# Optimization experiments

Measured on AMD Instinct MI355X. Metric: run time of the kernel, lower is better.

The kernel has to match this reference:

```python
import jax, jax.numpy as jnp
import numpy as np

H, D = 8, 8            # heads, per-head dim (hid_dim = 64)
HID = H * D
L = 6                  # HGTConv layers
NI, NV = 32768, 131072 # num 'instr' / 'var' nodes (batch_size == NI)
E_VV, E_VI, E_IV = 1048576, 524288, 524288
INV_SQRT_D = float(1.0 / np.sqrt(D))


def _seg_softmax(logits, seg, n):
    # softmax over edges grouped by destination node (PyG softmax semantics)
    m = jax.ops.segment_max(logits, seg, num_segments=n)
    m = jnp.where(jnp.isfinite(m), m, 0.0)
    e = jnp.exp(logits - m[seg])
    s = jax.ops.segment_sum(e, seg, num_segments=n)
    return e / (s[seg] + 1e-16)


def _edge_msg(k_src, v_src, q_dst, arel, mrel, prel, src, dst, n_dst):
    # relation-specific transforms: [N_src,H,D] x [H,D,D] -> [N_src,H,D]
    k_rel = jnp.einsum('nhd,hde->nhe', k_src, arel)
    v_rel = jnp.einsum('nhd,hde->nhe', v_src, mrel)
    alpha = jnp.einsum('ehd,ehd->eh', q_dst[dst], k_rel[src]) * prel * INV_SQRT_D  # [E,H]
    w = _seg_softmax(alpha, dst, n_dst)
    return jax.ops.segment_sum(v_rel[src] * w[:, :, None], dst, num_segments=n_dst)


def _kqv(x, Wk, Wq, Wv, bk, bq, bv, n):
    k = (x @ Wk.T + bk).reshape(n, H, D)
    q = (x @ Wq.T + bq).reshape(n, H, D)
    v = (x @ Wv.T + bv).reshape(n, H, D)
    return k, q, v


def _forward(x_instr, x_var,
             Wk_i, Wq_i, Wv_i, Wa_i, bk_i, bq_i, bv_i, ba_i, skip_i,
             Wk_v, Wq_v, Wv_v, Wa_v, bk_v, bq_v, bv_v, ba_v, skip_v,
             arel_vv, mrel_vv, prel_vv, arel_vi, mrel_vi, prel_vi,
             arel_iv, mrel_iv, prel_iv,
             Wqkv, bqkv, Wo, bo,
             mw0, mb0, mw1, mb1, mw2, mb2, mw3, mb3, mw4, mb4, mw5, mb5,
             src_vv, dst_vv, src_vi, dst_vi, src_iv, dst_iv):
    xi, xv = x_instr, x_var
    outs = []
    for l in range(L):
        k_i, q_i, v_i = _kqv(xi, Wk_i[l], Wq_i[l], Wv_i[l], bk_i[l], bq_i[l], bv_i[l], NI)
        k_v, q_v, v_v = _kqv(xv, Wk_v[l], Wq_v[l], Wv_v[l], bk_v[l], bq_v[l], bv_v[l], NV)
        # per-edge-type attention softmax + scatter-sum, then sum over edge types (group='sum')
        agg_v = (_edge_msg(k_v, v_v, q_v, arel_vv[l], mrel_vv[l], prel_vv[l], src_vv, dst_vv, NV)
                 + _edge_msg(k_i, v_i, q_v, arel_iv[l], mrel_iv[l], prel_iv[l], src_iv, dst_iv, NV))
        agg_i = _edge_msg(k_v, v_v, q_i, arel_vi[l], mrel_vi[l], prel_vi[l], src_vi, dst_vi, NI)
        o_i = jax.nn.gelu(agg_i.reshape(NI, HID), approximate=False) @ Wa_i[l].T + ba_i[l]
        b_i = jax.nn.sigmoid(skip_i[l])
        xi = b_i * o_i + (1.0 - b_i) * xi
        o_v = jax.nn.gelu(agg_v.reshape(NV, HID), approximate=False) @ Wa_v[l].T + ba_v[l]
        b_v = jax.nn.sigmoid(skip_v[l])
        xv = b_v * o_v + (1.0 - b_v) * xv
        if l > 0:
            outs.append(xi)
    # jumping-knowledge MultiheadAttention over the L-1 stacked layer outputs
    x = jnp.stack(outs)                        # [S, NI, HID], S = L-1 = 5
    S = x.shape[0]
    qkv = x @ Wqkv.T + bqkv                    # [S, NI, 3*HID]
    q, k, v = jnp.split(qkv, 3, axis=-1)
    q = q.reshape(S, NI, H, D)
    k = k.reshape(S, NI, H, D)
    v = v.reshape(S, NI, H, D)
    sc = jnp.einsum('snhd,tnhd->nhst', q, k) * INV_SQRT_D
    w = jax.nn.softmax(sc, axis=-1)
    o = jnp.einsum('nhst,tnhd->snhd', w, v).reshape(S, NI, HID)
    o = o @ Wo.T + bo
    out = o.sum(axis=0)                        # [NI, HID]; batch_size == NI so view is identity
    for W, b in ((mw0, mb0), (mw1, mb1), (mw2, mb2), (mw3, mb3), (mw4, mb4)):
        out = jax.nn.gelu(out @ W.T + b, approximate=False)
    out = out @ mw5.T + mb5                    # [NI, 1]
    return out[:, 0]


def setup_inputs() -> dict:
    key = jax.random.key(0)
    ks = iter(jax.random.split(key, 64))
    def nrm(shape, scale=1.0):
        return jax.random.normal(next(ks), shape, dtype=jnp.float32) * scale
    d = {}
    d['x_instr'] = nrm((NI, HID))
    d['x_var'] = nrm((NV, HID))
    for t in ('i', 'v'):
        for p in ('Wk', 'Wq', 'Wv', 'Wa'):
            d[f'{p}_{t}'] = nrm((L, HID, HID), (2.0 / HID) ** 0.5)
        for p in ('bk', 'bq', 'bv', 'ba'):
            d[f'{p}_{t}'] = jnp.zeros((L, HID), jnp.float32)
        d[f'skip_{t}'] = jnp.ones((L,), jnp.float32)
    for e in ('vv', 'vi', 'iv'):
        d[f'arel_{e}'] = nrm((L, H, D, D), (1.0 / D) ** 0.5)
        d[f'mrel_{e}'] = nrm((L, H, D, D), (1.0 / D) ** 0.5)
        d[f'prel_{e}'] = jnp.ones((L, H), jnp.float32)
    d['Wqkv'] = nrm((3 * HID, HID), (2.0 / HID) ** 0.5)
    d['bqkv'] = jnp.zeros((3 * HID,), jnp.float32)
    d['Wo'] = nrm((HID, HID), (2.0 / HID) ** 0.5)
    d['bo'] = jnp.zeros((HID,), jnp.float32)
    dims = [64, 32, 16, 8, 4, 2, 1]
    for i in range(6):
        d[f'mw{i}'] = nrm((dims[i + 1], dims[i]), (2.0 / dims[i]) ** 0.5)
        d[f'mb{i}'] = jnp.zeros((dims[i + 1],), jnp.float32)
    d['src_vv'] = jax.random.randint(next(ks), (E_VV,), 0, NV, dtype=jnp.int32).astype(jnp.int64)
    d['dst_vv'] = jax.random.randint(next(ks), (E_VV,), 0, NV, dtype=jnp.int32).astype(jnp.int64)
    d['src_vi'] = jax.random.randint(next(ks), (E_VI,), 0, NV, dtype=jnp.int32).astype(jnp.int64)
    d['dst_vi'] = jax.random.randint(next(ks), (E_VI,), 0, NI, dtype=jnp.int32).astype(jnp.int64)
    d['src_iv'] = jax.random.randint(next(ks), (E_IV,), 0, NI, dtype=jnp.int32).astype(jnp.int64)
    d['dst_iv'] = jax.random.randint(next(ks), (E_IV,), 0, NV, dtype=jnp.int32).astype(jnp.int64)
    return d


def reference(x_instr, x_var,
              Wk_i, Wq_i, Wv_i, Wa_i, bk_i, bq_i, bv_i, ba_i, skip_i,
              Wk_v, Wq_v, Wv_v, Wa_v, bk_v, bq_v, bv_v, ba_v, skip_v,
              arel_vv, mrel_vv, prel_vv, arel_vi, mrel_vi, prel_vi,
              arel_iv, mrel_iv, prel_iv,
              Wqkv, bqkv, Wo, bo,
              mw0, mb0, mw1, mb1, mw2, mb2, mw3, mb3, mw4, mb4, mw5, mb5,
              src_vv, dst_vv, src_vi, dst_vi, src_iv, dst_iv):
    return _forward(x_instr, x_var,
                    Wk_i, Wq_i, Wv_i, Wa_i, bk_i, bq_i, bv_i, ba_i, skip_i,
                    Wk_v, Wq_v, Wv_v, Wa_v, bk_v, bq_v, bv_v, ba_v, skip_v,
                    arel_vv, mrel_vv, prel_vv, arel_vi, mrel_vi, prel_vi,
                    arel_iv, mrel_iv, prel_iv,
                    Wqkv, bqkv, Wo, bo,
                    mw0, mb0, mw1, mb1, mw2, mb2, mw3, mb3, mw4, mb4, mw5, mb5,
                    src_vv, dst_vv, src_vi, dst_vi, src_iv, dst_iv)
```

## Files before the change

kernel.cpp:

```cpp
#include <hip/hip_runtime.h>
#include <cmath>

typedef _Float16 f16_t;
typedef __attribute__((ext_vector_type(8))) short short8;
typedef __attribute__((ext_vector_type(8))) _Float16 half8;
typedef __attribute__((ext_vector_type(4))) float f32x4;
typedef _Float16 h2v __attribute__((ext_vector_type(2)));
typedef _Float16 h8 __attribute__((ext_vector_type(8)));
typedef float f2 __attribute__((ext_vector_type(2)));

#define NI_N 32768
#define NV_N 131072
#define E_VV 1048576
#define E_VI 524288
#define E_IV 524288
#define NT_N (NV_N+NV_N+NI_N)
#define ET_N (E_VV+E_IV+E_VI)
#define SC_WIN 4
#define LOG2E 1.4426950408889634f
#define CHV 192
#define CHI 64
#define CHQ 256
#define EPAD 68

__device__ __forceinline__ float gelu_f(float x){ return 0.5f*x*(1.0f+erff(x*0.7071067811865476f)); }

__device__ __forceinline__ void splitf16(float v, short& hi, short& lo){
  f16_t h=(f16_t)v;
  hi=__builtin_bit_cast(short,h);
  f16_t l=(f16_t)(v-(float)h);
  lo=__builtin_bit_cast(short,l);
}
__device__ __forceinline__ f32x4 mfma16(short8 a, short8 b, f32x4 c){
  return __builtin_amdgcn_mfma_f32_16x16x32_f16(__builtin_bit_cast(half8,a),__builtin_bit_cast(half8,b),c,0,0,0);
}
__device__ __forceinline__ float fexp2(float x){
#if __has_builtin(__builtin_amdgcn_exp2f)
  return __builtin_amdgcn_exp2f(x);
#else
  return exp2f(x);
#endif
}
__device__ __forceinline__ float ldval(const float* p){ return *p; }
__device__ __forceinline__ float ldval(const f16_t* p){ return (float)*p; }
__device__ __forceinline__ void stval(float* p,float v){ *p=v; }
__device__ __forceinline__ void stval(f16_t* p,float v){ *p=(f16_t)v; }

__global__ __launch_bounds__(256) void k_hist3(const int* __restrict__ dvv,const int* __restrict__ div_,
    const int* __restrict__ dvi,int* __restrict__ cnt){
  int i=blockIdx.x*256+threadIdx.x;
  if(i<E_VV) atomicAdd(&cnt[dvv[i]],1);
  else if(i<E_VV+E_IV) atomicAdd(&cnt[NV_N+div_[i-E_VV]],1);
  else atomicAdd(&cnt[2*NV_N+dvi[i-E_VV-E_IV]],1);
}
__global__ __launch_bounds__(512) void k_scan1(const int* __restrict__ cnt,int N,int* __restrict__ rp,int* __restrict__ bsum){
  __shared__ int sh[512];
  int i=blockIdx.x*512+threadIdx.x;
  int v=(i<N)?cnt[i]:0;
  sh[threadIdx.x]=v; __syncthreads();
  for(int off=1;off<512;off<<=1){
    int t=(threadIdx.x>=(unsigned)off)?sh[threadIdx.x-off]:0; __syncthreads();
    sh[threadIdx.x]+=t; __syncthreads();
  }
  if(i<N) rp[i]=sh[threadIdx.x]-v;
  if(threadIdx.x==511) bsum[blockIdx.x]=sh[511];
}
__global__ __launch_bounds__(1024) void k_scan2(const int* __restrict__ bsum,int* __restrict__ boff,int nb){
  __shared__ int sh[1024];
  int t=threadIdx.x;
  int v=(t<nb)?bsum[t]:0;
  sh[t]=v; __syncthreads();
  for(int off=1;off<1024;off<<=1){
    int x=(t>=(unsigned)off)?sh[t-off]:0; __syncthreads();
    sh[t]+=x; __syncthreads();
  }
  if(t<nb) boff[t]=sh[t]-v;
  if(t==1023) boff[nb]=sh[1023];
}
__global__ __launch_bounds__(512) void k_scan3(int* __restrict__ rp,const int* __restrict__ boff,int* __restrict__ cur,int N,int nb){
  int i=blockIdx.x*512+threadIdx.x;
  if(i<N){ int v=rp[i]+boff[i>>9]; rp[i]=v; cur[i]=v; }
  if(i==0) rp[N]=boff[nb];
}
__global__ __launch_bounds__(256) void k_scatter3w(const int* __restrict__ svv,const int* __restrict__ dvv,
    const int* __restrict__ siv,const int* __restrict__ div_,
    const int* __restrict__ svi,const int* __restrict__ dvi,
    int* __restrict__ cur,int* __restrict__ esrc,int dlo,int dhi){
  int i=blockIdx.x*256+threadIdx.x;
  int d,s;
  if(i<E_VV){ d=dvv[i]; if(d<dlo||d>=dhi) return; s=svv[i]*320; }
  else if(i<E_VV+E_IV){ int j=i-E_VV; d=NV_N+div_[j]; if(d<dlo||d>=dhi) return; s=siv[j]*192; }
  else { int j=i-E_VV-E_IV; d=2*NV_N+dvi[j]; if(d<dlo||d>=dhi) return; s=svi[j]*320; }
  int p=atomicAdd(&cur[d],1); esrc[p]=s;
}

__global__ __launch_bounds__(256) void k_castx(const float* __restrict__ xi_in,const float* __restrict__ xv_in,
    f16_t* __restrict__ xi,f16_t* __restrict__ xv){
  int i=blockIdx.x*256+threadIdx.x;
  if(i<NI_N*64) xi[i]=(f16_t)xi_in[i];
  else { int j=i-NI_N*64; xv[j]=(f16_t)xv_in[j]; }
}

struct FoldArgs{
  const float *Wk_i,*Wq_i,*Wv_i,*bk_i,*bq_i,*bv_i;
  const float *Wk_v,*Wq_v,*Wv_v,*bk_v,*bq_v,*bv_v;
  const float *arel_vv,*mrel_vv,*prel_vv,*arel_vi,*mrel_vi,*prel_vi,*arel_iv,*mrel_iv,*prel_iv;
  const float *Wa_i,*Wa_v;
  short *fwh_var,*fwl_var,*fwh_ins,*fwl_ins,*wah_i,*wal_i,*wah_v,*wal_v;
  float *fwb_var,*fwb_ins;
};
__global__ __launch_bounds__(256) void k_fold6(FoldArgs fa){
  int gid=blockIdx.x*256+threadIdx.x;
  if(gid>=6*640*64) return;
  int l=gid/(640*64);
  int rem=gid-l*640*64;
  int r=rem>>6, c=rem&63;
  if(r>=512){
    int ro=r&63;
    const float* W=(r<576)?fa.Wa_i:fa.Wa_v;
    short *sh=((r<576)?fa.wah_i:fa.wah_v)+l*4096, *sl=((r<576)?fa.wal_i:fa.wal_v)+l*4096;
    short h,lo; splitf16(W[l*4096+ro*64+c],h,lo);
    sh[ro*64+c]=h; sl[ro*64+c]=lo;
    return;
  }
  const float *W,*B,*rel=nullptr,*prl=nullptr;
  short *sh,*sl; float *fwb; int orow; bool isq=false;
  if(r<320){
    sh=fa.fwh_var+l*320*64; sl=fa.fwl_var+l*320*64; fwb=fa.fwb_var+l*320; orow=r;
    if(r<64){ W=fa.Wq_v; B=fa.bq_v; isq=true; }
    else if(r<128){ W=fa.Wk_v; B=fa.bk_v; rel=fa.arel_vv; prl=fa.prel_vv; }
    else if(r<192){ W=fa.Wv_v; B=fa.bv_v; rel=fa.mrel_vv; }
    else if(r<256){ W=fa.Wk_v; B=fa.bk_v; rel=fa.arel_vi; prl=fa.prel_vi; }
    else         { W=fa.Wv_v; B=fa.bv_v; rel=fa.mrel_vi; }
  }else{
    int rr=r-320; sh=fa.fwh_ins+l*192*64; sl=fa.fwl_ins+l*192*64; fwb=fa.fwb_ins+l*192; orow=rr;
    if(rr<64){ W=fa.Wq_i; B=fa.bq_i; isq=true; }
    else if(rr<128){ W=fa.Wk_i; B=fa.bk_i; rel=fa.arel_iv; prl=fa.prel_iv; }
    else           { W=fa.Wv_i; B=fa.bv_i; rel=fa.mrel_iv; }
  }
  int d=orow&63;
  float val,bval;
  if(!rel){
    val=W[l*4096+d*64+c]; bval=B[l*64+d];
  }else{
    int h=d>>3, e=d&7;
    float s=prl?prl[l*8+h]*0.3535533905932738f:1.0f;
    float acc=0.f,bacc=0.f;
    #pragma unroll
    for(int dd=0;dd<8;dd++){
      float rv=rel[l*512+h*64+dd*8+e];
      acc += W[l*4096+(h*8+dd)*64+c]*rv;
      bacc+= B[l*64+h*8+dd]*rv;
    }
    val=acc*s; bval=bacc*s;
  }
  if(isq){ val*=LOG2E; bval*=LOG2E; }
  short h2q,lo2; splitf16(val,h2q,lo2);
  sh[orow*64+c]=h2q; sl[orow*64+c]=lo2;
  if(c==0) fwb[orow]=bval;
}

__global__ __launch_bounds__(256) void k_split2(const float* __restrict__ W,int n,short* __restrict__ hi,short* __restrict__ lo){
  int i=blockIdx.x*256+threadIdx.x;
  if(i<n){ short h,l2; splitf16(W[i],h,l2); hi[i]=h; lo[i]=l2; }
}

__device__ __forceinline__ void colres_body(const f16_t* __restrict__ A,int nrb,
    const short* __restrict__ Bh,const short* __restrict__ Bl,
    const float* __restrict__ bias,f16_t* __restrict__ out,int octot,int ocol0,
    int c,int CH,int wave,int lane,int m,int quad,f16_t (*rep)[72])
{
  short8 bhi[4][2], blo[4][2]; float bb[4];
  #pragma unroll
  for(int ot=0;ot<4;ot++){
    size_t o=(size_t)(ocol0+ot*16+m)*64+quad*8;
    bhi[ot][0]=*(const short8*)(Bh+o);    bhi[ot][1]=*(const short8*)(Bh+o+32);
    blo[ot][0]=*(const short8*)(Bl+o);    blo[ot][1]=*(const short8*)(Bl+o+32);
    bb[ot]=bias[ocol0+ot*16+m];
  }
  int rr0=lane>>3, seg=lane&7;
  for(int rb=c;rb<nrb;rb+=CH){
    int row0=rb*64+wave*16;
    const f16_t* ap=A+(size_t)(row0+m)*64+quad*8;
    short8 a0=*(const short8*)(const void*)ap;
    short8 a1=*(const short8*)(const void*)(ap+32);
    f32x4 acc[4];
    #pragma unroll
    for(int ot=0;ot<4;ot++){ f32x4 t={bb[ot],bb[ot],bb[ot],bb[ot]}; acc[ot]=t; }
    #pragma unroll
    for(int ot=0;ot<4;ot++){
      acc[ot]=mfma16(a0,blo[ot][0],acc[ot]);
      acc[ot]=mfma16(a0,bhi[ot][0],acc[ot]);
      acc[ot]=mfma16(a1,blo[ot][1],acc[ot]);
      acc[ot]=mfma16(a1,bhi[ot][1],acc[ot]);
    }
    #pragma unroll
    for(int ot=0;ot<4;ot++)
      #pragma unroll
      for(int r=0;r<4;r++)
        rep[quad*4+r][ot*16+m]=(f16_t)acc[ot][r];
    #pragma unroll
    for(int it=0;it<2;it++){
      int rr=it*8+rr0;
      h8 vals=*(const h8*)&rep[rr][seg*8];
      *(h8*)(out+(size_t)(row0+rr)*octot+ocol0+seg*8)=vals;
    }
  }
}

__global__ __launch_bounds__(256) void k_colres_feat(const f16_t* __restrict__ Av,const f16_t* __restrict__ Ai,
    const short* __restrict__ Bvh,const short* __restrict__ Bvl,const float* __restrict__ biasv,
    const short* __restrict__ Bih,const short* __restrict__ Bil,const float* __restrict__ biasi,
    f16_t* __restrict__ outv,f16_t* __restrict__ outi)
{
  __shared__ f16_t rep[4][16][72];
  const int wave=threadIdx.x>>6, lane=threadIdx.x&63;
  const int m=lane&15, quad=lane>>4;
  int bx=blockIdx.x;
  if(bx<5*CHV){
    int pan=bx/CHV, c=bx%CHV;
    colres_body(Av,NV_N/64,Bvh,Bvl,biasv,outv,320,pan*64,c,CHV,wave,lane,m,quad,rep[wave]);
  }else{
    bx-=5*CHV;
    int pan=bx/CHI, c=bx%CHI;
    colres_body(Ai,NI_N/64,Bih,Bil,biasi,outi,192,pan*64,c,CHI,wave,lane,m,quad,rep[wave]);
  }
}

__global__ __launch_bounds__(256) void k_colres1(const f16_t* __restrict__ A,int nrb,
    const short* __restrict__ Bh,const short* __restrict__ Bl,
    const float* __restrict__ bias,f16_t* __restrict__ out,int octot,int CH)
{
  __shared__ f16_t rep[4][16][72];
  const int wave=threadIdx.x>>6, lane=threadIdx.x&63;
  const int m=lane&15, quad=lane>>4;
  int pan=blockIdx.x/CH, c=blockIdx.x%CH;
  colres_body(A,nrb,Bh,Bl,bias,out,octot,pan*64,c,CH,wave,lane,m,quad,rep[wave]);
}

template<typename AT, typename OT>
__device__ __forceinline__ void gemm_body(const AT* __restrict__ A,int row0,
    const short* __restrict__ Bh,const short* __restrict__ Bl,
    const float* __restrict__ bias,float bias_scale,
    OT* __restrict__ out,int octot,int ocol0,int npanels,int m,int quad,int lane,
    f16_t (*rep)[72])
{
  const AT* ap=A+(size_t)(row0+m)*64+quad*8;
  constexpr bool AF16 = (sizeof(AT)==2);
  short8 ahi[2], alo[2];
  if constexpr(AF16){
    #pragma unroll
    for(int kf=0;kf<2;kf++) ahi[kf]=*(const short8*)(const void*)(ap+kf*32);
  }else{
    #pragma unroll
    for(int kf=0;kf<2;kf++){
      short8 th,tl;
      #pragma unroll
      for(int j=0;j<8;j++){ short h,l2; splitf16(ldval(&ap[kf*32+j]),h,l2); th[j]=h; tl[j]=l2; }
      ahi[kf]=th; alo[kf]=tl;
    }
  }
  for(int pan=0;pan<npanels;pan++){
    int colbase=pan*64;
    short8 bhi[4][2], blo[4][2];
    #pragma unroll
    for(int ot=0;ot<4;ot++){
      size_t o=(size_t)(colbase+ot*16+m)*64+quad*8;
      #pragma unroll
      for(int kf=0;kf<2;kf++){
        bhi[ot][kf]=*(const short8*)(Bh+o+kf*32);
        blo[ot][kf]=*(const short8*)(Bl+o+kf*32);
      }
    }
    f32x4 acc[4];
    #pragma unroll
    for(int ot=0;ot<4;ot++){
      float bv=bias[colbase+ot*16+m]*bias_scale;
      acc[ot][0]=bv; acc[ot][1]=bv; acc[ot][2]=bv; acc[ot][3]=bv;
    }
    #pragma unroll
    for(int ot=0;ot<4;ot++){
      #pragma unroll
      for(int kf=0;kf<2;kf++){
        if constexpr(!AF16) acc[ot]=mfma16(alo[kf],bhi[ot][kf],acc[ot]);
        acc[ot]=mfma16(ahi[kf],blo[ot][kf],acc[ot]);
        acc[ot]=mfma16(ahi[kf],bhi[ot][kf],acc[ot]);
      }
    }
    if constexpr(sizeof(OT)==2){
      #pragma unroll
      for(int ot=0;ot<4;ot++)
        #pragma unroll
        for(int r=0;r<4;r++)
          rep[quad*4+r][ot*16+m]=(f16_t)acc[ot][r];
      #pragma unroll
      for(int it=0;it<2;it++){
        int rr=it*8+(lane>>3), seg=lane&7;
        h8 vals=*(const h8*)&rep[rr][seg*8];
        *(h8*)(out+(size_t)(row0+rr)*octot+ocol0+colbase+seg*8)=vals;
      }
    }else{
      #pragma unroll
      for(int ot=0;ot<4;ot++){
        int col=ocol0+colbase+ot*16+m;
        #pragma unroll
        for(int r=0;r<4;r++){
          int row=row0+quad*4+r;
          stval(&out[(size_t)row*octot+col],acc[ot][r]);
        }
      }
    }
  }
}

template<typename AT, typename OT>
__global__ __launch_bounds__(256) void k_gemm64p(const AT* __restrict__ A,int N,
    const short* __restrict__ Bh,const short* __restrict__ Bl,
    const float* __restrict__ bias,float bias_scale,
    OT* __restrict__ out,int octot,int ocol0,int npanels)
{
  __shared__ f16_t rep[4][16][72];
  const int wave=threadIdx.x>>6, lane=threadIdx.x&63;
  const int m=lane&15, quad=lane>>4;
  const int row0=blockIdx.x*64+wave*16;
  if(row0>=N) return;
  gemm_body<AT,OT>(A,row0,Bh,Bl,bias,bias_scale,out,octot,ocol0,npanels,m,quad,lane,rep[wave]);
}

__global__ __launch_bounds__(256) void k_update2(const f16_t* __restrict__ agg_i,const f16_t* __restrict__ agg_v,
    const short* __restrict__ wah_i,const short* __restrict__ wal_i,
    const short* __restrict__ wah_v,const short* __restrict__ wal_v,
    const float* __restrict__ ba_i,const float* __restrict__ ba_v,
    const float* __restrict__ skip_i,const float* __restrict__ skip_v,
    f16_t* __restrict__ x_i,f16_t* __restrict__ x_v,
    f16_t* __restrict__ outs,int nbi)
{
  __shared__ f16_t rep[4][16][72];
  const int wave=threadIdx.x>>6, lane=threadIdx.x&63;
  const int m=lane&15, quad=lane>>4;
  const bool isI=(int)blockIdx.x<nbi;
  const int row0=(isI?blockIdx.x:(blockIdx.x-nbi))*64+wave*16;
  const f16_t* agg=isI?agg_i:agg_v;
  const short* Wah=isI?wah_i:wah_v;
  const short* Wal=isI?wal_i:wal_v;
  const float* ba=isI?ba_i:ba_v;
  const float* skip=isI?skip_i:skip_v;
  f16_t* x=isI?x_i:x_v;
  f16_t* oo=isI?outs:nullptr;
  f16_t (*R)[72]=rep[wave];
  short8 bhi[4][2], blo[4][2];
  #pragma unroll
  for(int ot=0;ot<4;ot++){
    size_t o=(size_t)(ot*16+m)*64+quad*8;
    #pragma unroll
    for(int kf=0;kf<2;kf++){
      bhi[ot][kf]=*(const short8*)(Wah+o+kf*32);
      blo[ot][kf]=*(const short8*)(Wal+o+kf*32);
    }
  }
  const f16_t* ap=agg+(size_t)(row0+m)*64+quad*8;
  short8 ahi[2], alo[2];
  #pragma unroll
  for(int kf=0;kf<2;kf++){
    short8 th,tl;
    #pragma unroll
    for(int j=0;j<8;j++){ short h,l2; splitf16(gelu_f((float)ap[kf*32+j]),h,l2); th[j]=h; tl[j]=l2; }
    ahi[kf]=th; alo[kf]=tl;
  }
  int rr0=lane>>3, seg=lane&7;
  h8 x0=*(const h8*)(x+(size_t)(row0+rr0)*64+seg*8);
  h8 x1=*(const h8*)(x+(size_t)(row0+8+rr0)*64+seg*8);
  *(h8*)&R[rr0][seg*8]=x0;
  *(h8*)&R[8+rr0][seg*8]=x1;
  f32x4 acc[4];
  #pragma unroll
  for(int ot=0;ot<4;ot++){
    float bv=ba[ot*16+m];
    acc[ot][0]=bv; acc[ot][1]=bv; acc[ot][2]=bv; acc[ot][3]=bv;
  }
  #pragma unroll
  for(int ot=0;ot<4;ot++){
    #pragma unroll
    for(int kf=0;kf<2;kf++){
      acc[ot]=mfma16(alo[kf],bhi[ot][kf],acc[ot]);
      acc[ot]=mfma16(ahi[kf],blo[ot][kf],acc[ot]);
      acc[ot]=mfma16(ahi[kf],bhi[ot][kf],acc[ot]);
    }
  }
  float s=1.0f/(1.0f+__expf(-skip[0]));
  #pragma unroll
  for(int ot=0;ot<4;ot++){
    int col=ot*16+m;
    #pragma unroll
    for(int r=0;r<4;r++){
      int row=quad*4+r;
      float xn=s*acc[ot][r]+(1.0f-s)*(float)R[row][col];
      R[row][col]=(f16_t)xn;
    }
  }
  h8 o0=*(const h8*)&R[rr0][seg*8];
  h8 o1=*(const h8*)&R[8+rr0][seg*8];
  *(h8*)(x+(size_t)(row0+rr0)*64+seg*8)=o0;
  *(h8*)(x+(size_t)(row0+8+rr0)*64+seg*8)=o1;
  if(oo){
    *(h8*)(oo+(size_t)(row0+rr0)*64+seg*8)=o0;
    *(h8*)(oo+(size_t)(row0+8+rr0)*64+seg*8)=o1;
  }
}

__device__ __forceinline__ float dot8(h8 k,h2v q0,h2v q1,h2v q2,h2v q3){
#if __has_builtin(__builtin_amdgcn_fdot2)
  float p=__builtin_amdgcn_fdot2((h2v){k[0],k[1]},q0,0.f,false);
  p=__builtin_amdgcn_fdot2((h2v){k[2],k[3]},q1,p,false);
  p=__builtin_amdgcn_fdot2((h2v){k[4],k[5]},q2,p,false);
  p=__builtin_amdgcn_fdot2((h2v){k[6],k[7]},q3,p,false);
  return p;
#else
  return (float)k[0]*(float)q0[0]+(float)k[1]*(float)q0[1]
        +(float)k[2]*(float)q1[0]+(float)k[3]*(float)q1[1]
        +(float)k[4]*(float)q2[0]+(float)k[5]*(float)q2[1]
        +(float)k[6]*(float)q3[0]+(float)k[7]*(float)q3[1];
#endif
}

__device__ __forceinline__ float edge_agg_eh(const int* __restrict__ rp,const int* __restrict__ es,
    const f16_t* __restrict__ sf,int koff,int voff,int n,int e_slot,int h,int lane,
    h2v q0,h2v q1,h2v q2,h2v q3,float* __restrict__ L)
{
  int b=__builtin_amdgcn_readfirstlane(rp[n]);
  int e=__builtin_amdgcn_readfirstlane(rp[n+1]);
  if(b==e) return 0.f;
  float m=-1e30f, ls=0.f;
  f2 A0={0.f,0.f},A1={0.f,0.f},A2={0.f,0.f},A3={0.f,0.f};
  const int hb=h*8;
  for(int i=b;i<e;i+=8){
    int eidx=i+e_slot;
    bool valid=eidx<e;
    int ec=valid?eidx:(e-1);
    int off=es[ec];
    const f16_t* kp=sf+(size_t)(unsigned)off+koff+hb;
    h8 kv=*(const h8*)kp;
    h8 vv=*(const h8*)(sf+(size_t)(unsigned)off+voff+hb);
    float p=dot8(kv,q0,q1,q2,q3);
    float d=p-m;
    if(__builtin_expect(d>8.f,0)){
      float sc=fexp2(-d);
      ls*=sc;
      f2 S={sc,sc};
      A0*=S; A1*=S; A2*=S; A3*=S;
      m=p; d=0.f;
    }
    float w=valid?fexp2(d):0.f;
    ls+=w;
    f2 W={w,w};
    A0+=W*(f2){(float)vv[0],(float)vv[1]};
    A1+=W*(f2){(float)vv[2],(float)vv[3]};
    A2+=W*(f2){(float)vv[4],(float)vv[5]};
    A3+=W*(f2){(float)vv[6],(float)vv[7]};
  }
  float mall=fmaxf(m,__shfl_xor(m,8));
  mall=fmaxf(mall,__shfl_xor(mall,16));
  mall=fmaxf(mall,__shfl_xor(mall,32));
  float scl=fexp2(m-mall);
  ls*=scl;
  float lsall=ls+__shfl_xor(ls,8);
  lsall+=__shfl_xor(lsall,16);
  lsall+=__shfl_xor(lsall,32);
  f2 S2={scl,scl};
  A0*=S2; A1*=S2; A2*=S2; A3*=S2;
  float* wp=L+e_slot*EPAD+hb;
  *(f32x4*)wp=(f32x4){A0[0],A0[1],A1[0],A1[1]};
  *(f32x4*)(wp+4)=(f32x4){A2[0],A2[1],A3[0],A3[1]};
  __asm__ volatile("s_waitcnt lgkmcnt(0)" ::: "memory");
  float r=0.f;
  #pragma unroll
  for(int ee=0;ee<8;ee++) r+=L[ee*EPAD+lane];
  float lsr=__shfl(lsall,lane>>3);
  return r/(lsr+1e-16f);
}

__global__ __launch_bounds__(256) void k_edge_all(const int* __restrict__ rp_all,const int* __restrict__ es,
    const f16_t* __restrict__ var_feat,const f16_t* __restrict__ ins_feat,
    f16_t* __restrict__ agg_v,f16_t* __restrict__ agg_i,int nbv)
{
  __shared__ float lds[4][8*EPAD];
  int wave=threadIdx.x>>6, lane=threadIdx.x&63;
  int e_slot=lane>>3, h=lane&7;
  float* L=lds[wave];
  if((int)blockIdx.x<nbv){
    int n=blockIdx.x*4+wave;
    const f16_t* qp=var_feat+(size_t)n*320+h*8;
    h8 qv=*(const h8*)qp;
    h2v q0={qv[0],qv[1]},q1={qv[2],qv[3]},q2={qv[4],qv[5]},q3={qv[6],qv[7]};
    float r1=edge_agg_eh(rp_all,es,var_feat,64,128,n,e_slot,h,lane,q0,q1,q2,q3,L);
    float r2=edge_agg_eh(rp_all+NV_N,es,ins_feat,64,128,n,e_slot,h,lane,q0,q1,q2,q3,L);
    agg_v[(size_t)n*64+lane]=(f16_t)(r1+r2);
  }else{
    int n=(blockIdx.x-nbv)*4+wave;
    const f16_t* qp=ins_feat+(size_t)n*192+h*8;
    h8 qv=*(const h8*)qp;
    h2v q0={qv[0],qv[1]},q1={qv[2],qv[3]},q2={qv[4],qv[5]},q3={qv[6],qv[7]};
    float r=edge_agg_eh(rp_all+2*NV_N,es,var_feat,192,256,n,e_slot,h,lane,q0,q1,q2,q3,L);
    agg_i[(size_t)n*64+lane]=(f16_t)r;
  }
}

__global__ __launch_bounds__(256) void k_jk(const f16_t* __restrict__ qkv,float* __restrict__ osum,int n_nodes){
  int wave=threadIdx.x>>6, lane=threadIdx.x&63;
  int n=blockIdx.x*4+wave;
  if(n>=n_nodes) return;
  float q[5],k[5],v[5];
  #pragma unroll
  for(int s=0;s<5;s++){
    const f16_t* p=qkv+((size_t)s*n_nodes+n)*192;
    q[s]=(float)p[lane]; k[s]=(float)p[64+lane]; v[s]=(float)p[128+lane];
  }
  float sc[5][5];
  #pragma unroll
  for(int s=0;s<5;s++)
    #pragma unroll
    for(int t=0;t<5;t++){
      float x=q[s]*k[t];
      x+=__shfl_xor(x,1); x+=__shfl_xor(x,2); x+=__shfl_xor(x,4);
      sc[s][t]=x*0.3535533905932738f;
    }
  float os=0.f;
  #pragma unroll
  for(int s=0;s<5;s++){
    float m=sc[s][0];
    #pragma unroll
    for(int t=1;t<5;t++) m=fmaxf(m,sc[s][t]);
    float den=0.f, acc=0.f;
    #pragma unroll
    for(int t=0;t<5;t++){ float e=__expf(sc[s][t]-m); den+=e; acc+=e*v[t]; }
    os+=acc/den;
  }
  osum[(size_t)n*64+lane]=os;
}

struct MlpArgs{ const float *w0,*b0,*w1,*b1,*w2,*b2,*w3,*b3,*w4,*b4,*w5,*b5; };
__global__ __launch_bounds__(256) void k_mlp(const float* __restrict__ in,MlpArgs ma,float* __restrict__ out,int N){
  __shared__ float sw0[2048],sb0[32],sw1[512],sb1[16],sw2[128],sb2[8],sw3[32],sb3[4],sw4[8],sb4[2],sw5[2],sb5[1];
  for(int i=threadIdx.x;i<2048;i+=256) sw0[i]=ma.w0[i];
  for(int i=threadIdx.x;i<512;i+=256)  sw1[i]=ma.w1[i];
  if(threadIdx.x<128) sw2[threadIdx.x]=ma.w2[threadIdx.x];
  if(threadIdx.x<32){ sb0[threadIdx.x]=ma.b0[threadIdx.x]; sw3[threadIdx.x]=ma.w3[threadIdx.x]; }
  if(threadIdx.x<16) sb1[threadIdx.x]=ma.b1[threadIdx.x];
  if(threadIdx.x<8){ sb2[threadIdx.x]=ma.b2[threadIdx.x]; sw4[threadIdx.x]=ma.w4[threadIdx.x]; }
  if(threadIdx.x<4) sb3[threadIdx.x]=ma.b3[threadIdx.x];
  if(threadIdx.x<2){ sb4[threadIdx.x]=ma.b4[threadIdx.x]; sw5[threadIdx.x]=ma.w5[threadIdx.x]; }
  if(threadIdx.x==0) sb5[0]=ma.b5[0];
  __syncthreads();
  int n=blockIdx.x*256+threadIdx.x;
  if(n>=N) return;
  float a[64];
  const f32x4* p4=(const f32x4*)(in+(size_t)n*64);
  #pragma unroll
  for(int j=0;j<16;j++){ f32x4 t=p4[j]; a[4*j]=t[0]; a[4*j+1]=t[1]; a[4*j+2]=t[2]; a[4*j+3]=t[3]; }
  float h1[32];
  #pragma unroll
  for(int o=0;o<32;o++){ float s=sb0[o];
    #pragma unroll
    for(int c=0;c<64;c++) s+=a[c]*sw0[o*64+c];
    h1[o]=gelu_f(s); }
  float h2q[16];
  #pragma unroll
  for(int o=0;o<16;o++){ float s=sb1[o];
    #pragma unroll
    for(int c=0;c<32;c++) s+=h1[c]*sw1[o*32+c];
    h2q[o]=gelu_f(s); }
  float h3[8];
  #pragma unroll
  for(int o=0;o<8;o++){ float s=sb2[o];
    #pragma unroll
    for(int c=0;c<16;c++) s+=h2q[c]*sw2[o*16+c];
    h3[o]=gelu_f(s); }
  float h4[4];
  #pragma unroll
  for(int o=0;o<4;o++){ float s=sb3[o];
    #pragma unroll
    for(int c=0;c<8;c++) s+=h3[c]*sw3[o*8+c];
    h4[o]=gelu_f(s); }
  float h5[2];
  #pragma unroll
  for(int o=0;o<2;o++){ float s=sb4[o];
    #pragma unroll
    for(int c=0;c<4;c++) s+=h4[c]*sw4[o*4+c];
    h5[o]=gelu_f(s); }
  float r=sb5[0]+h5[0]*sw5[0]+h5[1]*sw5[1];
  out[n]=r;
}

extern "C" void kernel_launch(void* const* d_in,const int* in_sizes,int n_in,
                              void* d_out,int out_size,void* d_ws,size_t ws_size,
                              hipStream_t stream){
  (void)in_sizes;(void)n_in;(void)out_size;(void)ws_size;
  const float* x_instr=(const float*)d_in[0];
  const float* x_var  =(const float*)d_in[1];
  const float* ba_i=(const float*)d_in[9];
  const float* skip_i=(const float*)d_in[10];
  const float* ba_v=(const float*)d_in[18];
  const float* skip_v=(const float*)d_in[19];
  const float* Wqkv=(const float*)d_in[29];
  const float* bqkv=(const float*)d_in[30];
  const float* Wo=(const float*)d_in[31];
  const float* bo=(const float*)d_in[32];
  const int* src_vv=(const int*)d_in[45];
  const int* dst_vv=(const int*)d_in[46];
  const int* src_vi=(const int*)d_in[47];
  const int* dst_vi=(const int*)d_in[48];
  const int* src_iv=(const int*)d_in[49];
  const int* dst_iv=(const int*)d_in[50];

  char* w=(char*)d_ws;
  auto alloc=[&](size_t b)->char*{ char* p=w; w+=(b+255)&~(size_t)255; return p; };
  int* rp_all=(int*)alloc((size_t)(NT_N+1)*4);
  int* cnt_all=(int*)alloc((size_t)NT_N*4);
  int* cur_all=(int*)alloc((size_t)NT_N*4);
  int* bsum =(int*)alloc(640*4);
  int* boff =(int*)alloc(640*4);
  int* esrc_all=(int*)alloc((size_t)ET_N*4);
  short* fwh_var=(short*)alloc((size_t)6*320*64*2);
  short* fwl_var=(short*)alloc((size_t)6*320*64*2);
  float* fwb_var=(float*)alloc((size_t)6*320*4);
  short* fwh_ins=(short*)alloc((size_t)6*192*64*2);
  short* fwl_ins=(short*)alloc((size_t)6*192*64*2);
  float* fwb_ins=(float*)alloc((size_t)6*192*4);
  short* wah_i=(short*)alloc((size_t)6*64*64*2);
  short* wal_i=(short*)alloc((size_t)6*64*64*2);
  short* wah_v=(short*)alloc((size_t)6*64*64*2);
  short* wal_v=(short*)alloc((size_t)6*64*64*2);
  short* qkvh=(short*)alloc(192*64*2);
  short* qkvl=(short*)alloc(192*64*2);
  short* woh=(short*)alloc(64*64*2);
  short* wol=(short*)alloc(64*64*2);
  f16_t* outs=(f16_t*)alloc((size_t)5*NI_N*64*2);
  char* arena=alloc((size_t)146800640);
  f16_t*  xv      =(f16_t*)(arena);
  f16_t*  xi      =(f16_t*)(arena+16777216);
  f16_t*  var_feat=(f16_t*)(arena+20971520);
  f16_t*  ins_feat=(f16_t*)(arena+104857600);
  f16_t*  agg_v   =(f16_t*)(arena+117440512);
  f16_t*  agg_i   =(f16_t*)(arena+134217728);
  f16_t*  qkv    =(f16_t*)(arena);
  float*  osum   =(float*)(arena+67108864);
  float*  out_jk =(float*)(arena+75497472);

  hipMemsetAsync(cnt_all,0,(size_t)NT_N*4,stream);
  k_hist3<<<ET_N/256,256,0,stream>>>(dst_vv,dst_iv,dst_vi,cnt_all);
  int nb=NT_N/512;
  k_scan1<<<nb,512,0,stream>>>(cnt_all,NT_N,rp_all,bsum);
  k_scan2<<<1,1024,0,stream>>>(bsum,boff,nb);
  k_scan3<<<nb,512,0,stream>>>(rp_all,boff,cur_all,NT_N,nb);
  for(int wdx=0;wdx<SC_WIN;wdx++){
    int dlo=wdx*(NT_N/SC_WIN), dhi=(wdx+1)*(NT_N/SC_WIN);
    k_scatter3w<<<ET_N/256,256,0,stream>>>(src_vv,dst_vv,src_iv,dst_iv,src_vi,dst_vi,cur_all,esrc_all,dlo,dhi);
  }

  k_castx<<<(NI_N*64+NV_N*64)/256,256,0,stream>>>(x_instr,x_var,xi,xv);

  k_split2<<<(192*64+255)/256,256,0,stream>>>(Wqkv,192*64,qkvh,qkvl);
  k_split2<<<(64*64+255)/256,256,0,stream>>>(Wo,64*64,woh,wol);

  FoldArgs fa;
  fa.Wk_i=(const float*)d_in[2]; fa.Wq_i=(const float*)d_in[3]; fa.Wv_i=(const float*)d_in[4];
  fa.bk_i=(const float*)d_in[6]; fa.bq_i=(const float*)d_in[7]; fa.bv_i=(const float*)d_in[8];
  fa.Wk_v=(const float*)d_in[11]; fa.Wq_v=(const float*)d_in[12]; fa.Wv_v=(const float*)d_in[13];
  fa.bk_v=(const float*)d_in[15]; fa.bq_v=(const float*)d_in[16]; fa.bv_v=(const float*)d_in[17];
  fa.arel_vv=(const float*)d_in[20]; fa.mrel_vv=(const float*)d_in[21]; fa.prel_vv=(const float*)d_in[22];
  fa.arel_vi=(const float*)d_in[23]; fa.mrel_vi=(const float*)d_in[24]; fa.prel_vi=(const float*)d_in[25];
  fa.arel_iv=(const float*)d_in[26]; fa.mrel_iv=(const float*)d_in[27]; fa.prel_iv=(const float*)d_in[28];
  fa.Wa_i=(const float*)d_in[5]; fa.Wa_v=(const float*)d_in[14];
  fa.fwh_var=fwh_var; fa.fwl_var=fwl_var; fa.fwh_ins=fwh_ins; fa.fwl_ins=fwl_ins;
  fa.wah_i=wah_i; fa.wal_i=wal_i; fa.wah_v=wah_v; fa.wal_v=wal_v;
  fa.fwb_var=fwb_var; fa.fwb_ins=fwb_ins;
  k_fold6<<<(6*640*64)/256,256,0,stream>>>(fa);

  for(int l=0;l<6;l++){
    k_colres_feat<<<5*CHV+3*CHI,256,0,stream>>>(xv,xi,
        fwh_var+(size_t)l*320*64,fwl_var+(size_t)l*320*64,fwb_var+l*320,
        fwh_ins+(size_t)l*192*64,fwl_ins+(size_t)l*192*64,fwb_ins+l*192,
        var_feat,ins_feat);
    k_edge_all<<<NV_N/4+NI_N/4,256,0,stream>>>(rp_all,esrc_all,var_feat,ins_feat,agg_v,agg_i,NV_N/4);
    k_update2<<<NI_N/64+NV_N/64,256,0,stream>>>(agg_i,agg_v,
        wah_i+(size_t)l*4096,wal_i+(size_t)l*4096,wah_v+(size_t)l*4096,wal_v+(size_t)l*4096,
        ba_i+l*64,ba_v+l*64,skip_i+l,skip_v+l,xi,xv,
        (l>0)?(outs+(size_t)(l-1)*NI_N*64):nullptr,NI_N/64);
  }

  k_colres1<<<3*CHQ,256,0,stream>>>(outs,5*NI_N/64,qkvh,qkvl,bqkv,qkv,192,CHQ);
  k_jk<<<NI_N/4,256,0,stream>>>(qkv,osum,NI_N);
  k_gemm64p<float,float><<<NI_N/64,256,0,stream>>>(osum,NI_N,woh,wol,bo,5.0f,out_jk,64,0,1);
  MlpArgs ma;
  ma.w0=(const float*)d_in[33]; ma.b0=(const float*)d_in[34];
  ma.w1=(const float*)d_in[35]; ma.b1=(const float*)d_in[36];
  ma.w2=(const float*)d_in[37]; ma.b2=(const float*)d_in[38];
  ma.w3=(const float*)d_in[39]; ma.b3=(const float*)d_in[40];
  ma.w4=(const float*)d_in[41]; ma.b4=(const float*)d_in[42];
  ma.w5=(const float*)d_in[43]; ma.b5=(const float*)d_in[44];
  k_mlp<<<NI_N/256,256,0,stream>>>(out_jk,ma,(float*)d_out,NI_N);
}
```

Before: 1.542 ms.

## Software-pipeline edge gathers and hoist first-chunk loads in edge aggregation kernel

Restructures the per-destination edge loop so the next chunk's edge-source index is prefetched while the current chunk is processed. The first chunk's key/value vectors for both var-destination relations are loaded up front, so their latencies overlap. It also replaces the conditional online-softmax rescale with a branch-free max/rescale per step, and halves the scatter window count in preprocessing. The cost is more registers and extra exp work per edge, which could reduce occupancy.

```diff
diff --git a/kernel.cpp b/kernel.cpp
--- a/kernel.cpp
+++ b/kernel.cpp
@@ -16,7 +16,7 @@
 #define E_IV 524288
 #define NT_N (NV_N+NV_N+NI_N)
 #define ET_N (E_VV+E_IV+E_VI)
-#define SC_WIN 4
+#define SC_WIN 2
 #define LOG2E 1.4426950408889634f
 #define CHV 192
 #define CHI 64
@@ -423,40 +423,52 @@
 #endif
 }
 
-__device__ __forceinline__ float edge_agg_eh(const int* __restrict__ rp,const int* __restrict__ es,
-    const f16_t* __restrict__ sf,int koff,int voff,int n,int e_slot,int h,int lane,
-    h2v q0,h2v q1,h2v q2,h2v q3,float* __restrict__ L)
+__device__ __forceinline__ float edge_body(int b,int e,const int* __restrict__ es,
+    const f16_t* __restrict__ sf,int koff,int e_slot,int lane,
+    h2v q0,h2v q1,h2v q2,h2v q3,float* __restrict__ L,h8 pk,h8 pv)
 {
-  int b=__builtin_amdgcn_readfirstlane(rp[n]);
-  int e=__builtin_amdgcn_readfirstlane(rp[n+1]);
-  if(b==e) return 0.f;
+  if(b>=e) return 0.f;
   float m=-1e30f, ls=0.f;
   f2 A0={0.f,0.f},A1={0.f,0.f},A2={0.f,0.f},A3={0.f,0.f};
-  const int hb=h*8;
-  for(int i=b;i<e;i+=8){
-    int eidx=i+e_slot;
-    bool valid=eidx<e;
-    int ec=valid?eidx:(e-1);
-    int off=es[ec];
+  const int hb=(lane&7)*8;
+  int off=0;
+  if(b+8<e){ int ec=b+8+e_slot; ec=ec<e?ec:e-1; off=es[ec]; }
+  {
+    bool valid=(b+e_slot)<e;
+    float p=dot8(pk,q0,q1,q2,q3);
+    p=valid?p:-1e30f;
+    float mn=fmaxf(m,p);
+    float sc=fexp2(m-mn);
+    float w=valid?fexp2(p-mn):0.f;
+    ls=fmaf(ls,sc,w);
+    f2 S={sc,sc},W={w,w};
+    A0=A0*S+W*(f2){(float)pv[0],(float)pv[1]};
+    A1=A1*S+W*(f2){(float)pv[2],(float)pv[3]};
+    A2=A2*S+W*(f2){(float)pv[4],(float)pv[5]};
+    A3=A3*S+W*(f2){(float)pv[6],(float)pv[7]};
+    m=mn;
+  }
+  for(int i=b+8;i<e;i+=8){
+    int inext=i+8;
+    int offn=0;
+    if(inext<e){ int ec=inext+e_slot; ec=ec<e?ec:e-1; offn=es[ec]; }
     const f16_t* kp=sf+(size_t)(unsigned)off+koff+hb;
     h8 kv=*(const h8*)kp;
-    h8 vv=*(const h8*)(sf+(size_t)(unsigned)off+voff+hb);
+    h8 vv=*(const h8*)(kp+64);
+    bool valid=(i+e_slot)<e;
     float p=dot8(kv,q0,q1,q2,q3);
-    float d=p-m;
-    if(__builtin_expect(d>8.f,0)){
-      float sc=fexp2(-d);
-      ls*=sc;
-      f2 S={sc,sc};
-      A0*=S; A1*=S; A2*=S; A3*=S;
-      m=p; d=0.f;
-    }
-    float w=valid?fexp2(d):0.f;
-    ls+=w;
-    f2 W={w,w};
-    A0+=W*(f2){(float)vv[0],(float)vv[1]};
-    A1+=W*(f2){(float)vv[2],(float)vv[3]};
-    A2+=W*(f2){(float)vv[4],(float)vv[5]};
-    A3+=W*(f2){(float)vv[6],(float)vv[7]};
+    p=valid?p:-1e30f;
+    float mn=fmaxf(m,p);
+    float sc=fexp2(m-mn);
+    float w=valid?fexp2(p-mn):0.f;
+    ls=fmaf(ls,sc,w);
+    f2 S={sc,sc},W={w,w};
+    A0=A0*S+W*(f2){(float)vv[0],(float)vv[1]};
+    A1=A1*S+W*(f2){(float)vv[2],(float)vv[3]};
+    A2=A2*S+W*(f2){(float)vv[4],(float)vv[5]};
+    A3=A3*S+W*(f2){(float)vv[6],(float)vv[7]};
+    m=mn;
+    off=offn;
   }
   float mall=fmaxf(m,__shfl_xor(m,8));
   mall=fmaxf(mall,__shfl_xor(mall,16));
@@ -485,22 +497,47 @@
 {
   __shared__ float lds[4][8*EPAD];
   int wave=threadIdx.x>>6, lane=threadIdx.x&63;
-  int e_slot=lane>>3, h=lane&7;
+  int e_slot=lane>>3, hb=(lane&7)*8;
   float* L=lds[wave];
   if((int)blockIdx.x<nbv){
     int n=blockIdx.x*4+wave;
-    const f16_t* qp=var_feat+(size_t)n*320+h*8;
-    h8 qv=*(const h8*)qp;
+    int b1=__builtin_amdgcn_readfirstlane(rp_all[n]);
+    int e1=__builtin_amdgcn_readfirstlane(rp_all[n+1]);
+    const int* rp2=rp_all+NV_N;
+    int b2=__builtin_amdgcn_readfirstlane(rp2[n]);
+    int e2=__builtin_amdgcn_readfirstlane(rp2[n+1]);
+    h8 qv=*(const h8*)(var_feat+(size_t)n*320+hb);
+    int off1=0,off2=0;
+    if(b1<e1){ int ec=b1+e_slot; ec=ec<e1?ec:e1-1; off1=es[ec]; }
+    if(b2<e2){ int ec=b2+e_slot; ec=ec<e2?ec:e2-1; off2=es[ec]; }
+    h8 pk1={},pv1={},pk2={},pv2={};
+    if(b1<e1){
+      const f16_t* p1=var_feat+(size_t)(unsigned)off1+64+hb;
+      pk1=*(const h8*)p1; pv1=*(const h8*)(p1+64);
+    }
+    if(b2<e2){
+      const f16_t* p2=ins_feat+(size_t)(unsigned)off2+64+hb;
+      pk2=*(const h8*)p2; pv2=*(const h8*)(p2+64);
+    }
     h2v q0={qv[0],qv[1]},q1={qv[2],qv[3]},q2={qv[4],qv[5]},q3={qv[6],qv[7]};
-    float r1=edge_agg_eh(rp_all,es,var_feat,64,128,n,e_slot,h,lane,q0,q1,q2,q3,L);
-    float r2=edge_agg_eh(rp_all+NV_N,es,ins_feat,64,128,n,e_slot,h,lane,q0,q1,q2,q3,L);
+    float r1=edge_body(b1,e1,es,var_feat,64,e_slot,lane,q0,q1,q2,q3,L,pk1,pv1);
+    float r2=edge_body(b2,e2,es,ins_feat,64,e_slot,lane,q0,q1,q2,q3,L,pk2,pv2);
     agg_v[(size_t)n*64+lane]=(f16_t)(r1+r2);
   }else{
-    int n=(blockIdx.x-nbv)*4+wave;
-    const f16_t* qp=ins_feat+(size_t)n*192+h*8;
-    h8 qv=*(const h8*)qp;
+    int n=((int)blockIdx.x-nbv)*4+wave;
+    const int* rp=rp_all+2*NV_N;
+    int b=__builtin_amdgcn_readfirstlane(rp[n]);
+    int e=__builtin_amdgcn_readfirstlane(rp[n+1]);
+    h8 qv=*(const h8*)(ins_feat+(size_t)n*192+hb);
+    int off0=0;
+    if(b<e){ int ec=b+e_slot; ec=ec<e?ec:e-1; off0=es[ec]; }
+    h8 pk={},pv={};
+    if(b<e){
+      const f16_t* p=var_feat+(size_t)(unsigned)off0+192+hb;
+      pk=*(const h8*)p; pv=*(const h8*)(p+64);
+    }
     h2v q0={qv[0],qv[1]},q1={qv[2],qv[3]},q2={qv[4],qv[5]},q3={qv[6],qv[7]};
-    float r=edge_agg_eh(rp_all+2*NV_N,es,var_feat,192,256,n,e_slot,h,lane,q0,q1,q2,q3,L);
+    float r=edge_body(b,e,es,var_feat,192,e_slot,lane,q0,q1,q2,q3,L,pk,pv);
     agg_i[(size_t)n*64+lane]=(f16_t)r;
   }
 }
@@ -669,7 +706,7 @@
   fa.bk_v=(const float*)d_in[15]; fa.bq_v=(const float*)d_in[16]; fa.bv_v=(const float*)d_in[17];
   fa.arel_vv=(const float*)d_in[20]; fa.mrel_vv=(const float*)d_in[21]; fa.prel_vv=(const float*)d_in[22];
   fa.arel_vi=(const float*)d_in[23]; fa.mrel_vi=(const float*)d_in[24]; fa.prel_vi=(const float*)d_in[25];
-  fa.arel_iv=(const float*)d_in[26]; fa.mrel_iv=(const float*)d_in[27]; fa.prel_iv=(const float*)d_in[28];
+  fa.arel_iv=(const float*)d_in[26]; fa.mrel_iv=(const float*)d_in[27]; fa.mrel_iv=(const float*)d_in[27]; fa.prel_iv=(const float*)d_in[28];
   fa.Wa_i=(const float*)d_in[5]; fa.Wa_v=(const float*)d_in[14];
   fa.fwh_var=fwh_var; fa.fwl_var=fwl_var; fa.fwh_ins=fwh_ins; fa.fwl_ins=fwl_ins;
   fa.wah_i=wah_i; fa.wal_i=wal_i; fa.wah_v=wah_v; fa.wal_v=wal_v;
```

Measured after the change: 1.479 ms. 1.04x faster.
